# Performance work log

Measured on AMD Instinct MI355X. Metric: run time of the kernel, lower is better.

Reference implementation:

```python
import jax, jax.numpy as jnp
import numpy as np

B, S, D, H = 2, 2048, 1024, 16
DK = D // H  # 64, even -> RoPE valid


def _rotate_half(x):
    # torch: stack((-x[...,1::2], x[...,::2]), -1).flatten(-2) -> interleaved
    x1 = x[..., 0::2]
    x2 = x[..., 1::2]
    return jnp.stack((-x2, x1), axis=-1).reshape(x.shape)


def _build_rope(seq_len, d_k, dtype=jnp.float32):
    inv_freq = 1.0 / (10000.0 ** (jnp.arange(0, d_k, 2, dtype=dtype) / d_k))
    pos = jnp.arange(seq_len, dtype=dtype)
    angles = pos[:, None] * inv_freq[None, :]  # [S, d_k/2]
    sin = jnp.repeat(jnp.sin(angles), 2, axis=-1)  # [S, d_k]
    cos = jnp.repeat(jnp.cos(angles), 2, axis=-1)
    return cos, sin


def _apply_rope(x, cos, sin):
    # x: [B, H, S, d_k]; cos/sin: [S, d_k]
    return x * cos[None, None] + _rotate_half(x) * sin[None, None]


def setup_inputs():
    key = jax.random.key(0)
    ks = jax.random.split(key, 11)
    s = 0.02
    inp = {
        'Q': jax.random.normal(ks[0], (B, S, D), jnp.float32),
        'K': jax.random.normal(ks[1], (B, S, D), jnp.float32),
        'V': jax.random.normal(ks[2], (B, S, D), jnp.float32),
        'Wq': jax.random.normal(ks[3], (D, D), jnp.float32) * s,
        'bq': jnp.zeros((D,), jnp.float32),
        'Wk': jax.random.normal(ks[4], (D, D), jnp.float32) * s,
        'bk': jnp.zeros((D,), jnp.float32),
        'Wv': jax.random.normal(ks[5], (D, D), jnp.float32) * s,
        'bv': jnp.zeros((D,), jnp.float32),
        'Wo': jax.random.normal(ks[6], (D, D), jnp.float32) * s,
        'bo': jnp.zeros((D,), jnp.float32),
        # causal mask, broadcast over batch
        'mask': jnp.broadcast_to(jnp.tril(jnp.ones((S, S), jnp.int32))[None, None], (B, 1, S, S)),
    }
    return inp


def reference(Q, K, V, Wq, bq, Wk, bk, Wv, bv, Wo, bo, mask):
    # projections (torch Linear: x @ W.T + b), split heads -> [B, H, S, d_k]
    def proj(x, W, b):
        return (x @ W.T + b).reshape(B, -1, H, DK).transpose(0, 2, 1, 3)

    q = proj(Q, Wq, bq)
    k = proj(K, Wk, bk)
    v = proj(V, Wv, bv)

    cos, sin = _build_rope(S, DK)
    q = _apply_rope(q, cos, sin)
    k = _apply_rope(k, cos, sin)

    scores = jnp.einsum('bhqd,bhkd->bhqk', q, k) / jnp.sqrt(jnp.float32(DK))
    scores = jnp.where(mask == 0, -jnp.inf, scores)
    attn = jax.nn.softmax(scores, axis=-1)  # dropout is identity in eval / p=0
    out = jnp.einsum('bhqk,bhkd->bhqd', attn, v)  # [B, H, S, d_k]
    out = out.transpose(0, 2, 1, 3).reshape(B, -1, D)
    out = out @ Wo.T + bo
    return out, attn
```

## Files before the change

### kernel.cpp

```cpp
#include <hip/hip_runtime.h>
#include <math.h>

namespace {
constexpr int Bn  = 2;
constexpr int Sn  = 2048;
constexpr int Dn  = 1024;
constexpr int Hn  = 16;
constexpr int DKn = 64;
constexpr int Mn  = Bn * Sn;
}

typedef __attribute__((ext_vector_type(8))) short short8;
typedef __attribute__((ext_vector_type(4))) float f32x4;
typedef __attribute__((ext_vector_type(8))) unsigned short ushort8v;

__device__ __forceinline__ unsigned short f2bf(float x) {
  union { float f; unsigned u; } un; un.f = x;
  unsigned r = un.u + 0x7fffu + ((un.u >> 16) & 1u);
  return (unsigned short)(r >> 16);
}

__device__ __forceinline__ void async_copy16(const void* g, void* l) {
  __builtin_amdgcn_global_load_lds(
      (const __attribute__((address_space(1))) unsigned int*)g,
      (__attribute__((address_space(3))) unsigned int*)l, 16, 0, 0);
}

__device__ __forceinline__ int swz(int row, int ch) {
  return row * 64 + (((ch) ^ (row & 7)) << 3);
}

__global__ __launch_bounds__(256)
void cvt_bf16_kernel(const float* s0, const float* s1, const float* s2,
                     const float* s3, const float* s4, const float* s5,
                     const float* s6,
                     unsigned short* d0, unsigned short* d1, unsigned short* d2,
                     unsigned short* d3, unsigned short* d4, unsigned short* d5,
                     unsigned short* d6) {
  const int which = blockIdx.y;
  const float* s;
  unsigned short* d;
  int n;
  switch (which) {
    case 0: s = s0; d = d0; n = Mn * Dn; break;
    case 1: s = s1; d = d1; n = Mn * Dn; break;
    case 2: s = s2; d = d2; n = Mn * Dn; break;
    case 3: s = s3; d = d3; n = Dn * Dn; break;
    case 4: s = s4; d = d4; n = Dn * Dn; break;
    case 5: s = s5; d = d5; n = Dn * Dn; break;
    default: s = s6; d = d6; n = Dn * Dn; break;
  }
  int idx = (blockIdx.x * 256 + threadIdx.x) * 4;
  if (idx >= n) return;
  float4 v = *(const float4*)(s + idx);
  ushort4 o;
  o.x = f2bf(v.x); o.y = f2bf(v.y); o.z = f2bf(v.z); o.w = f2bf(v.w);
  *(ushort4*)(d + idx) = o;
}

__global__ void rope_table_kernel(float* __restrict__ cost, float* __restrict__ sint) {
  int s = blockIdx.x;
  int i = threadIdx.x;
  double inv_freq = pow(10000.0, -(double)(2 * i) / 64.0);
  double ang = (double)s * inv_freq;
  cost[s * 32 + i] = (float)cos(ang);
  sint[s * 32 + i] = (float)sin(ang);
}

__device__ __forceinline__ void gemm_bf16_core(const unsigned short* __restrict__ A,
                                               const unsigned short* __restrict__ B,
                                               int m0, int n0, int K, int tid,
                                               f32x4 (&acc)[4][4]) {
  __shared__ unsigned short As[128 * 32];
  __shared__ unsigned short Bs[128 * 32];
  const int lane = tid & 63, wave = tid >> 6;
  const int wrow = (wave >> 1) * 64, wcol = (wave & 1) * 64;
  const int lx = lane & 15, quad = lane >> 4;

  for (int k0 = 0; k0 < K; k0 += 32) {
    __syncthreads();
#pragma unroll
    for (int c = 0; c < 2; ++c) {
      int slot = wave * 128 + c * 64 + lane;
      int row = slot >> 2, ch = slot & 3;
      async_copy16(A + (size_t)(m0 + row) * K + k0 + ch * 8,
                   &As[(size_t)(wave * 128 + c * 64) * 8]);
      async_copy16(B + (size_t)(n0 + row) * K + k0 + ch * 8,
                   &Bs[(size_t)(wave * 128 + c * 64) * 8]);
    }
    __syncthreads();
    short8 af[4], bf[4];
#pragma unroll
    for (int i = 0; i < 4; ++i)
      af[i] = *(const short8*)&As[(wrow + i * 16 + lx) * 32 + quad * 8];
#pragma unroll
    for (int j = 0; j < 4; ++j)
      bf[j] = *(const short8*)&Bs[(wcol + j * 16 + lx) * 32 + quad * 8];
#pragma unroll
    for (int i = 0; i < 4; ++i)
#pragma unroll
      for (int j = 0; j < 4; ++j)
        acc[i][j] = __builtin_amdgcn_mfma_f32_16x16x32_bf16(af[i], bf[j], acc[i][j], 0, 0, 0);
  }
}

__global__ __launch_bounds__(256)
void qkv_mfma_kernel(const unsigned short* __restrict__ Xq,
                     const unsigned short* __restrict__ Xk,
                     const unsigned short* __restrict__ Xv,
                     const unsigned short* __restrict__ Wqb,
                     const unsigned short* __restrict__ Wkb,
                     const unsigned short* __restrict__ Wvb,
                     const float* __restrict__ bq, const float* __restrict__ bk,
                     const float* __restrict__ bv,
                     const float* __restrict__ cost, const float* __restrict__ sint,
                     unsigned short* __restrict__ qb, unsigned short* __restrict__ kb,
                     unsigned short* __restrict__ vb) {
  const int which = blockIdx.z;
  const unsigned short* A  = which == 0 ? Xq  : which == 1 ? Xk  : Xv;
  const unsigned short* Bw = which == 0 ? Wqb : which == 1 ? Wkb : Wvb;
  const float* bias        = which == 0 ? bq  : which == 1 ? bk  : bv;
  unsigned short* outp     = which == 0 ? qb  : which == 1 ? kb  : vb;
  const int m0 = blockIdx.x * 128, n0 = blockIdx.y * 128;
  const int tid = threadIdx.x, lane = tid & 63, wave = tid >> 6;
  const int wrow = (wave >> 1) * 64, wcol = (wave & 1) * 64;
  const int lx = lane & 15, quad = lane >> 4;

  f32x4 acc[4][4];
#pragma unroll
  for (int i = 0; i < 4; ++i)
#pragma unroll
    for (int j = 0; j < 4; ++j) acc[i][j] = (f32x4){0.f, 0.f, 0.f, 0.f};

  gemm_bf16_core(A, Bw, m0, n0, 1024, tid, acc);

#pragma unroll
  for (int ni = 0; ni < 4; ++ni) {
    const int gn = n0 + wcol + ni * 16 + lx;
    const int h = gn >> 6, dk = gn & 63;
    const float bb = bias[gn];
    const int pi = dk >> 1;
    const float sgn = (dk & 1) ? 1.f : -1.f;
#pragma unroll
    for (int mi = 0; mi < 4; ++mi) {
#pragma unroll
      for (int r = 0; r < 4; ++r) {
        const int gm = m0 + wrow + mi * 16 + quad * 4 + r;
        const int b = gm >> 11, spos = gm & 2047;
        float v = acc[mi][ni][r] + bb;
        if (which < 2) {
          float partner = __shfl_xor(v, 1, 64);
          float c = cost[spos * 32 + pi], s = sint[spos * 32 + pi];
          v = v * c + sgn * partner * s;
        }
        outp[((size_t)(b * Hn + h) * Sn + spos) * DKn + dk] = f2bf(v);
      }
    }
  }
}

__global__ __launch_bounds__(256)
void attn_mfma_kernel(const unsigned short* __restrict__ qb,
                      const unsigned short* __restrict__ kb,
                      const unsigned short* __restrict__ vb,
                      float* __restrict__ attn_out, unsigned short* __restrict__ ob) {
  const int qt = 31 - blockIdx.x;
  const int h = blockIdx.y, b = blockIdx.z;
  const size_t hoff = (size_t)(b * Hn + h) * Sn * DKn;
  const unsigned short* Qh = qb + hoff + (size_t)qt * 64 * 64;
  const unsigned short* Kh = kb + hoff;
  const unsigned short* Vh = vb + hoff;
  float* attn = attn_out + (size_t)(b * Hn + h) * Sn * Sn;

  __shared__ unsigned short qs[64 * 64];
  __shared__ unsigned short ks[64 * 64];
  __shared__ unsigned short vt[64 * 64];
  __shared__ unsigned short ps[64 * 64];

  const int tid = threadIdx.x, lane = tid & 63, wave = tid >> 6;
  const int quad = lane >> 4, lx = lane & 15;
  const int r0 = qt * 64;
  const float scale = 0.125f;

#pragma unroll
  for (int it = 0; it < 2; ++it) {
    int e = it * 256 + tid;
    int row = e >> 3, ch = e & 7;
    *(float4*)&qs[swz(row, ch)] = *(const float4*)(Qh + row * 64 + ch * 8);
  }
  __syncthreads();

  short8 aq[2];
  const int qrow = wave * 16 + lx;
#pragma unroll
  for (int ksc = 0; ksc < 2; ++ksc)
    aq[ksc] = *(const short8*)&qs[swz(qrow, quad + ksc * 4)];

  float lsum[4] = {0.f, 0.f, 0.f, 0.f};
  for (int kt = 0; kt <= qt; ++kt) {
    __syncthreads();
#pragma unroll
    for (int it = 0; it < 2; ++it) {
      int e = it * 256 + tid;
      int row = e >> 3, ch = e & 7;
      *(float4*)&ks[swz(row, ch)] =
          *(const float4*)(Kh + (size_t)(kt * 64 + row) * 64 + ch * 8);
    }
    __syncthreads();
#pragma unroll
    for (int c = 0; c < 4; ++c) {
      f32x4 s4 = (f32x4){0.f, 0.f, 0.f, 0.f};
      const int krow = c * 16 + lx;
#pragma unroll
      for (int ksc = 0; ksc < 2; ++ksc) {
        short8 bk8 = *(const short8*)&ks[swz(krow, quad + ksc * 4)];
        s4 = __builtin_amdgcn_mfma_f32_16x16x32_bf16(aq[ksc], bk8, s4, 0, 0, 0);
      }
      const int ct = c * 16 + lx;
#pragma unroll
      for (int r = 0; r < 4; ++r) {
        const int rt = wave * 16 + quad * 4 + r;
        float p = (kt == qt && ct > rt) ? 0.f : __expf(s4[r] * scale);
        lsum[r] += p;
      }
    }
  }
#pragma unroll
  for (int off = 1; off < 16; off <<= 1)
#pragma unroll
    for (int r = 0; r < 4; ++r) lsum[r] += __shfl_xor(lsum[r], off, 64);
  float inv_l[4];
#pragma unroll
  for (int r = 0; r < 4; ++r) inv_l[r] = 1.f / lsum[r];

  f32x4 oacc[4];
#pragma unroll
  for (int c = 0; c < 4; ++c) oacc[c] = (f32x4){0.f, 0.f, 0.f, 0.f};

  for (int kt = 0; kt <= qt; ++kt) {
    __syncthreads();
#pragma unroll
    for (int it = 0; it < 2; ++it) {
      int e = it * 256 + tid;
      int row = e >> 3, ch = e & 7;
      *(float4*)&ks[swz(row, ch)] =
          *(const float4*)(Kh + (size_t)(kt * 64 + row) * 64 + ch * 8);
      ushort8v vv = *(const ushort8v*)(Vh + (size_t)(kt * 64 + row) * 64 + ch * 8);
#pragma unroll
      for (int j = 0; j < 8; ++j) {
        int dk = ch * 8 + j;
        vt[dk * 64 + (((row >> 3) ^ (dk & 7)) << 3) + (row & 7)] = vv[j];
      }
    }
    __syncthreads();

#pragma unroll
    for (int c = 0; c < 4; ++c) {
      f32x4 s4 = (f32x4){0.f, 0.f, 0.f, 0.f};
      const int krow = c * 16 + lx;
#pragma unroll
      for (int ksc = 0; ksc < 2; ++ksc) {
        short8 bk8 = *(const short8*)&ks[swz(krow, quad + ksc * 4)];
        s4 = __builtin_amdgcn_mfma_f32_16x16x32_bf16(aq[ksc], bk8, s4, 0, 0, 0);
      }
      const int ct = c * 16 + lx;
      const int pch = (ct >> 3);
#pragma unroll
      for (int r = 0; r < 4; ++r) {
        const int rt = wave * 16 + quad * 4 + r;
        float p = (kt == qt && ct > rt) ? 0.f : __expf(s4[r] * scale) * inv_l[r];
        attn[(size_t)(r0 + rt) * Sn + kt * 64 + ct] = p;
        ps[rt * 64 + ((pch ^ (rt & 7)) << 3) + (ct & 7)] = f2bf(p);
      }
    }
    __syncthreads();

    short8 ap[2];
#pragma unroll
    for (int ksc = 0; ksc < 2; ++ksc)
      ap[ksc] = *(const short8*)&ps[swz(qrow, quad + ksc * 4)];
#pragma unroll
    for (int c2 = 0; c2 < 4; ++c2) {
      const int vrow = c2 * 16 + lx;
#pragma unroll
      for (int ksc = 0; ksc < 2; ++ksc) {
        short8 bv8 = *(const short8*)&vt[swz(vrow, quad + ksc * 4)];
        oacc[c2] = __builtin_amdgcn_mfma_f32_16x16x32_bf16(ap[ksc], bv8, oacc[c2], 0, 0, 0);
      }
    }
  }

#pragma unroll
  for (int c2 = 0; c2 < 4; ++c2) {
#pragma unroll
    for (int r = 0; r < 4; ++r) {
      const int grow = r0 + wave * 16 + quad * 4 + r;
      const int dk = c2 * 16 + lx;
      ob[((size_t)(b * Sn) + grow) * Dn + h * 64 + dk] = f2bf(oacc[c2][r]);
    }
  }

  const float4 z = make_float4(0.f, 0.f, 0.f, 0.f);
  for (int kt = qt + 1; kt < 32; ++kt) {
#pragma unroll
    for (int it = 0; it < 4; ++it) {
      int e = it * 256 + tid;
      int row = e >> 4, c4 = e & 15;
      *(float4*)(attn + (size_t)(r0 + row) * Sn + kt * 64 + c4 * 4) = z;
    }
  }
}

__global__ __launch_bounds__(256)
void outproj_mfma_kernel(const unsigned short* __restrict__ Ob,
                         const unsigned short* __restrict__ Wob,
                         const float* __restrict__ bo, float* __restrict__ out) {
  const int m0 = blockIdx.x * 128, n0 = blockIdx.y * 128;
  const int tid = threadIdx.x, lane = tid & 63, wave = tid >> 6;
  const int wrow = (wave >> 1) * 64, wcol = (wave & 1) * 64;
  const int lx = lane & 15, quad = lane >> 4;

  f32x4 acc[4][4];
#pragma unroll
  for (int i = 0; i < 4; ++i)
#pragma unroll
    for (int j = 0; j < 4; ++j) acc[i][j] = (f32x4){0.f, 0.f, 0.f, 0.f};

  gemm_bf16_core(Ob, Wob, m0, n0, 1024, tid, acc);

#pragma unroll
  for (int ni = 0; ni < 4; ++ni) {
    const int gn = n0 + wcol + ni * 16 + lx;
    const float bb = bo[gn];
#pragma unroll
    for (int mi = 0; mi < 4; ++mi) {
#pragma unroll
      for (int r = 0; r < 4; ++r) {
        const int gm = m0 + wrow + mi * 16 + quad * 4 + r;
        out[(size_t)gm * Dn + gn] = acc[mi][ni][r] + bb;
      }
    }
  }
}

extern "C" void kernel_launch(void* const* d_in, const int* in_sizes, int n_in,
                              void* d_out, int out_size, void* d_ws, size_t ws_size,
                              hipStream_t stream) {
  (void)in_sizes; (void)n_in; (void)out_size; (void)ws_size;
  const float* Q  = (const float*)d_in[0];
  const float* K  = (const float*)d_in[1];
  const float* V  = (const float*)d_in[2];
  const float* Wq = (const float*)d_in[3];
  const float* bq = (const float*)d_in[4];
  const float* Wk = (const float*)d_in[5];
  const float* bk = (const float*)d_in[6];
  const float* Wv = (const float*)d_in[7];
  const float* bv = (const float*)d_in[8];
  const float* Wo = (const float*)d_in[9];
  const float* bo = (const float*)d_in[10];

  float* out  = (float*)d_out;
  float* attn = out + (size_t)Mn * Dn;

  unsigned short* w = (unsigned short*)d_ws;
  unsigned short* Xqb = w;
  unsigned short* Xkb = Xqb + (size_t)Mn * Dn;
  unsigned short* Xvb = Xkb + (size_t)Mn * Dn;
  unsigned short* Wqb = Xvb + (size_t)Mn * Dn;
  unsigned short* Wkb = Wqb + (size_t)Dn * Dn;
  unsigned short* Wvb = Wkb + (size_t)Dn * Dn;
  unsigned short* Wob = Wvb + (size_t)Dn * Dn;
  unsigned short* qb  = Wob + (size_t)Dn * Dn;
  unsigned short* kb  = qb + (size_t)Mn * Dn;
  unsigned short* vb  = kb + (size_t)Mn * Dn;
  unsigned short* ob  = vb + (size_t)Mn * Dn;
  float* cost = (float*)(ob + (size_t)Mn * Dn);
  float* sint = cost + (size_t)Sn * 32;

  cvt_bf16_kernel<<<dim3(4096, 7), dim3(256), 0, stream>>>(
      Q, K, V, Wq, Wk, Wv, Wo, Xqb, Xkb, Xvb, Wqb, Wkb, Wvb, Wob);
  rope_table_kernel<<<dim3(Sn), dim3(32), 0, stream>>>(cost, sint);
  qkv_mfma_kernel<<<dim3(32, 8, 3), dim3(256), 0, stream>>>(
      Xqb, Xkb, Xvb, Wqb, Wkb, Wvb, bq, bk, bv, cost, sint, qb, kb, vb);
  attn_mfma_kernel<<<dim3(32, Hn, Bn), dim3(256), 0, stream>>>(qb, kb, vb, attn, ob);
  outproj_mfma_kernel<<<dim3(32, 8), dim3(256), 0, stream>>>(ob, Wob, bo, out);
}
```

Before: 832.3 us.

## Write V transposed from QKV GEMM and read K/V directly from global in attention

```diff
diff --git a/kernel.cpp b/kernel.cpp
--- a/kernel.cpp
+++ b/kernel.cpp
@@ -115,17 +115,19 @@
                      const float* __restrict__ bv,
                      const float* __restrict__ cost, const float* __restrict__ sint,
                      unsigned short* __restrict__ qb, unsigned short* __restrict__ kb,
-                     unsigned short* __restrict__ vb) {
+                     unsigned short* __restrict__ vtb) {
   const int which = blockIdx.z;
   const unsigned short* A  = which == 0 ? Xq  : which == 1 ? Xk  : Xv;
   const unsigned short* Bw = which == 0 ? Wqb : which == 1 ? Wkb : Wvb;
   const float* bias        = which == 0 ? bq  : which == 1 ? bk  : bv;
-  unsigned short* outp     = which == 0 ? qb  : which == 1 ? kb  : vb;
+  unsigned short* outp     = which == 0 ? qb  : which == 1 ? kb  : vtb;
   const int m0 = blockIdx.x * 128, n0 = blockIdx.y * 128;
   const int tid = threadIdx.x, lane = tid & 63, wave = tid >> 6;
   const int wrow = (wave >> 1) * 64, wcol = (wave & 1) * 64;
   const int lx = lane & 15, quad = lane >> 4;
 
+  __shared__ unsigned short tb[32][136];
+
   f32x4 acc[4][4];
 #pragma unroll
   for (int i = 0; i < 4; ++i)
@@ -134,26 +136,60 @@
 
   gemm_bf16_core(A, Bw, m0, n0, 1024, tid, acc);
 
-#pragma unroll
-  for (int ni = 0; ni < 4; ++ni) {
-    const int gn = n0 + wcol + ni * 16 + lx;
-    const int h = gn >> 6, dk = gn & 63;
-    const float bb = bias[gn];
-    const int pi = dk >> 1;
-    const float sgn = (dk & 1) ? 1.f : -1.f;
-#pragma unroll
-    for (int mi = 0; mi < 4; ++mi) {
-#pragma unroll
-      for (int r = 0; r < 4; ++r) {
-        const int gm = m0 + wrow + mi * 16 + quad * 4 + r;
-        const int b = gm >> 11, spos = gm & 2047;
-        float v = acc[mi][ni][r] + bb;
-        if (which < 2) {
+  if (which < 2) {
+#pragma unroll
+    for (int ni = 0; ni < 4; ++ni) {
+      const int gn = n0 + wcol + ni * 16 + lx;
+      const int h = gn >> 6, dk = gn & 63;
+      const float bb = bias[gn];
+      const int pi = dk >> 1;
+      const float sgn = (dk & 1) ? 1.f : -1.f;
+#pragma unroll
+      for (int mi = 0; mi < 4; ++mi) {
+#pragma unroll
+        for (int r = 0; r < 4; ++r) {
+          const int gm = m0 + wrow + mi * 16 + quad * 4 + r;
+          const int b = gm >> 11, spos = gm & 2047;
+          float v = acc[mi][ni][r] + bb;
           float partner = __shfl_xor(v, 1, 64);
           float c = cost[spos * 32 + pi], s = sint[spos * 32 + pi];
           v = v * c + sgn * partner * s;
+          outp[((size_t)(b * Hn + h) * Sn + spos) * DKn + dk] = f2bf(v);
         }
-        outp[((size_t)(b * Hn + h) * Sn + spos) * DKn + dk] = f2bf(v);
+      }
+    }
+  } else {
+    const int bb_ = m0 >> 11;
+    const int sp0 = m0 & 2047;
+#pragma unroll
+    for (int s = 0; s < 4; ++s) {
+      __syncthreads();
+      const bool mine = (wcol == 0) ? (s < 2) : (s >= 2);
+      if (mine) {
+        const int nia = (s & 1) * 2;
+#pragma unroll
+        for (int np = 0; np < 2; ++np) {
+          const int ni = nia + np;
+          const int fl = np * 16 + lx;
+          const float bbv = bias[n0 + s * 32 + fl];
+#pragma unroll
+          for (int mi = 0; mi < 4; ++mi)
+#pragma unroll
+            for (int r = 0; r < 4; ++r) {
+              const int tok = wrow + mi * 16 + quad * 4 + r;
+              tb[fl][tok] = f2bf(acc[mi][ni][r] + bbv);
+            }
+        }
+      }
+      __syncthreads();
+#pragma unroll
+      for (int it = 0; it < 2; ++it) {
+        const int e = it * 256 + tid;
+        const int f = e >> 4, ch = e & 15;
+        const int gn = n0 + s * 32 + f;
+        const int hh = gn >> 6, dk = gn & 63;
+        ushort8v val = *(const ushort8v*)&tb[f][ch * 8];
+        *(ushort8v*)(outp + ((size_t)(bb_ * Hn + hh) * DKn + dk) * Sn + sp0 + ch * 8) = val;
       }
     }
   }
@@ -162,58 +198,42 @@
 __global__ __launch_bounds__(256)
 void attn_mfma_kernel(const unsigned short* __restrict__ qb,
                       const unsigned short* __restrict__ kb,
-                      const unsigned short* __restrict__ vb,
+                      const unsigned short* __restrict__ vtb,
                       float* __restrict__ attn_out, unsigned short* __restrict__ ob) {
-  const int qt = 31 - blockIdx.x;
-  const int h = blockIdx.y, b = blockIdx.z;
-  const size_t hoff = (size_t)(b * Hn + h) * Sn * DKn;
-  const unsigned short* Qh = qb + hoff + (size_t)qt * 64 * 64;
-  const unsigned short* Kh = kb + hoff;
-  const unsigned short* Vh = vb + hoff;
-  float* attn = attn_out + (size_t)(b * Hn + h) * Sn * Sn;
-
-  __shared__ unsigned short qs[64 * 64];
-  __shared__ unsigned short ks[64 * 64];
-  __shared__ unsigned short vt[64 * 64];
+  const int wg = blockIdx.x;
+  const int xcd = wg & 7, j = wg >> 3;
+  const int bh = xcd * 4 + (j >> 5);
+  const int qt = 31 - (j & 31);
+  const int b = bh >> 4, h = bh & 15;
+  const size_t hoff = (size_t)bh * (Sn * DKn);
+  const unsigned short* Qh  = qb  + hoff + (size_t)qt * 64 * DKn;
+  const unsigned short* Kh  = kb  + hoff;
+  const unsigned short* VTh = vtb + hoff;
+  float* attn = attn_out + (size_t)bh * Sn * Sn;
+
   __shared__ unsigned short ps[64 * 64];
 
   const int tid = threadIdx.x, lane = tid & 63, wave = tid >> 6;
   const int quad = lane >> 4, lx = lane & 15;
   const int r0 = qt * 64;
   const float scale = 0.125f;
-
-#pragma unroll
-  for (int it = 0; it < 2; ++it) {
-    int e = it * 256 + tid;
-    int row = e >> 3, ch = e & 7;
-    *(float4*)&qs[swz(row, ch)] = *(const float4*)(Qh + row * 64 + ch * 8);
-  }
-  __syncthreads();
+  const int qrow = wave * 16 + lx;
 
   short8 aq[2];
-  const int qrow = wave * 16 + lx;
 #pragma unroll
   for (int ksc = 0; ksc < 2; ++ksc)
-    aq[ksc] = *(const short8*)&qs[swz(qrow, quad + ksc * 4)];
+    aq[ksc] = *(const short8*)(Qh + (size_t)qrow * DKn + (ksc * 4 + quad) * 8);
 
   float lsum[4] = {0.f, 0.f, 0.f, 0.f};
   for (int kt = 0; kt <= qt; ++kt) {
-    __syncthreads();
-#pragma unroll
-    for (int it = 0; it < 2; ++it) {
-      int e = it * 256 + tid;
-      int row = e >> 3, ch = e & 7;
-      *(float4*)&ks[swz(row, ch)] =
-          *(const float4*)(Kh + (size_t)(kt * 64 + row) * 64 + ch * 8);
-    }
-    __syncthreads();
 #pragma unroll
     for (int c = 0; c < 4; ++c) {
+      if (kt == qt && c > wave) continue;
       f32x4 s4 = (f32x4){0.f, 0.f, 0.f, 0.f};
-      const int krow = c * 16 + lx;
+      const int krow = kt * 64 + c * 16 + lx;
 #pragma unroll
       for (int ksc = 0; ksc < 2; ++ksc) {
-        short8 bk8 = *(const short8*)&ks[swz(krow, quad + ksc * 4)];
+        short8 bk8 = *(const short8*)(Kh + (size_t)krow * DKn + (ksc * 4 + quad) * 8);
         s4 = __builtin_amdgcn_mfma_f32_16x16x32_bf16(aq[ksc], bk8, s4, 0, 0, 0);
       }
       const int ct = c * 16 + lx;
@@ -238,29 +258,13 @@
   for (int c = 0; c < 4; ++c) oacc[c] = (f32x4){0.f, 0.f, 0.f, 0.f};
 
   for (int kt = 0; kt <= qt; ++kt) {
-    __syncthreads();
-#pragma unroll
-    for (int it = 0; it < 2; ++it) {
-      int e = it * 256 + tid;
-      int row = e >> 3, ch = e & 7;
-      *(float4*)&ks[swz(row, ch)] =
-          *(const float4*)(Kh + (size_t)(kt * 64 + row) * 64 + ch * 8);
-      ushort8v vv = *(const ushort8v*)(Vh + (size_t)(kt * 64 + row) * 64 + ch * 8);
-#pragma unroll
-      for (int j = 0; j < 8; ++j) {
-        int dk = ch * 8 + j;
-        vt[dk * 64 + (((row >> 3) ^ (dk & 7)) << 3) + (row & 7)] = vv[j];
-      }
-    }
-    __syncthreads();
-
 #pragma unroll
     for (int c = 0; c < 4; ++c) {
       f32x4 s4 = (f32x4){0.f, 0.f, 0.f, 0.f};
-      const int krow = c * 16 + lx;
+      const int krow = kt * 64 + c * 16 + lx;
 #pragma unroll
       for (int ksc = 0; ksc < 2; ++ksc) {
-        short8 bk8 = *(const short8*)&ks[swz(krow, quad + ksc * 4)];
+        short8 bk8 = *(const short8*)(Kh + (size_t)krow * DKn + (ksc * 4 + quad) * 8);
         s4 = __builtin_amdgcn_mfma_f32_16x16x32_bf16(aq[ksc], bk8, s4, 0, 0, 0);
       }
       const int ct = c * 16 + lx;
@@ -269,11 +273,12 @@
       for (int r = 0; r < 4; ++r) {
         const int rt = wave * 16 + quad * 4 + r;
         float p = (kt == qt && ct > rt) ? 0.f : __expf(s4[r] * scale) * inv_l[r];
-        attn[(size_t)(r0 + rt) * Sn + kt * 64 + ct] = p;
+        __builtin_nontemporal_store(p, &attn[(size_t)(r0 + rt) * Sn + kt * 64 + ct]);
         ps[rt * 64 + ((pch ^ (rt & 7)) << 3) + (ct & 7)] = f2bf(p);
       }
     }
-    __syncthreads();
+    asm volatile("s_waitcnt lgkmcnt(0)" ::: "memory");
+    __builtin_amdgcn_sched_barrier(0);
 
     short8 ap[2];
 #pragma unroll
@@ -284,7 +289,7 @@
       const int vrow = c2 * 16 + lx;
 #pragma unroll
       for (int ksc = 0; ksc < 2; ++ksc) {
-        short8 bv8 = *(const short8*)&vt[swz(vrow, quad + ksc * 4)];
+        short8 bv8 = *(const short8*)(VTh + (size_t)vrow * Sn + kt * 64 + ksc * 32 + quad * 8);
         oacc[c2] = __builtin_amdgcn_mfma_f32_16x16x32_bf16(ap[ksc], bv8, oacc[c2], 0, 0, 0);
       }
     }
@@ -300,13 +305,14 @@
     }
   }
 
-  const float4 z = make_float4(0.f, 0.f, 0.f, 0.f);
+  const f32x4 z = (f32x4){0.f, 0.f, 0.f, 0.f};
   for (int kt = qt + 1; kt < 32; ++kt) {
 #pragma unroll
     for (int it = 0; it < 4; ++it) {
       int e = it * 256 + tid;
       int row = e >> 4, c4 = e & 15;
-      *(float4*)(attn + (size_t)(r0 + row) * Sn + kt * 64 + c4 * 4) = z;
+      __builtin_nontemporal_store(
+          z, (f32x4*)(attn + (size_t)(r0 + row) * Sn + kt * 64 + c4 * 4));
     }
   }
 }
@@ -372,8 +378,8 @@
   unsigned short* Wob = Wvb + (size_t)Dn * Dn;
   unsigned short* qb  = Wob + (size_t)Dn * Dn;
   unsigned short* kb  = qb + (size_t)Mn * Dn;
-  unsigned short* vb  = kb + (size_t)Mn * Dn;
-  unsigned short* ob  = vb + (size_t)Mn * Dn;
+  unsigned short* vtb = kb + (size_t)Mn * Dn;
+  unsigned short* ob  = vtb + (size_t)Mn * Dn;
   float* cost = (float*)(ob + (size_t)Mn * Dn);
   float* sint = cost + (size_t)Sn * 32;
 
@@ -381,7 +387,7 @@
       Q, K, V, Wq, Wk, Wv, Wo, Xqb, Xkb, Xvb, Wqb, Wkb, Wvb, Wob);
   rope_table_kernel<<<dim3(Sn), dim3(32), 0, stream>>>(cost, sint);
   qkv_mfma_kernel<<<dim3(32, 8, 3), dim3(256), 0, stream>>>(
-      Xqb, Xkb, Xvb, Wqb, Wkb, Wvb, bq, bk, bv, cost, sint, qb, kb, vb);
-  attn_mfma_kernel<<<dim3(32, Hn, Bn), dim3(256), 0, stream>>>(qb, kb, vb, attn, ob);
+      Xqb, Xkb, Xvb, Wqb, Wkb, Wvb, bq, bk, bv, cost, sint, qb, kb, vtb);
+  attn_mfma_kernel<<<dim3(1024), dim3(256), 0, stream>>>(qb, kb, vtb, attn, ob);
   outproj_mfma_kernel<<<dim3(32, 8), dim3(256), 0, stream>>>(ob, Wob, bo, out);
 }
```

New measurement: 888.0 us. 1.07x slower.
